# Kernel optimization log

Hardware: AMD Instinct MI355X
Metric: run time of the kernel (lower is better)

Reference implementation:

```python
import jax, jax.numpy as jnp
import numpy as np
from jax import lax

B, N, NUM_CLASSES = 16, 48384, 1
CONF_THRESH = 0.25
IOU_THRESH = 0.45
MAX_PER_IMG = 100
K = 512           # NMS candidate pool (top-K by score)
IMG_SIZE = 1536.0
CLS_OFFSET = 4096.0  # class-aware NMS offset trick


def setup_inputs() -> dict:
    key = jax.random.key(0)
    k1, k2, k3 = jax.random.split(key, 3)
    # cx, cy in [0, IMG), w, h in [0, 0.2*IMG)
    coords = jax.random.uniform(k1, (B, N, 4)) * jnp.array(
        [IMG_SIZE, IMG_SIZE, 0.2 * IMG_SIZE, 0.2 * IMG_SIZE], dtype=jnp.float32)
    confs = jax.random.uniform(k2, (B, N, 1 + NUM_CLASSES))  # obj + class scores in [0,1)
    pred_boxes = jnp.concatenate([coords, confs], axis=-1)   # [B, N, 6]
    features = jax.random.normal(k3, (B, 256, 48, 48), dtype=jnp.float32)
    return {"pred_boxes": pred_boxes, "features": features}


def _iou_matrix(boxes):
    # boxes: [K, 4] xyxy -> [K, K] pairwise IoU
    area = jnp.clip(boxes[:, 2] - boxes[:, 0], 0.0) * jnp.clip(boxes[:, 3] - boxes[:, 1], 0.0)
    lt = jnp.maximum(boxes[:, None, :2], boxes[None, :, :2])
    rb = jnp.minimum(boxes[:, None, 2:], boxes[None, :, 2:])
    wh = jnp.clip(rb - lt, 0.0)
    inter = wh[..., 0] * wh[..., 1]
    return inter / (area[:, None] + area[None, :] - inter + 1e-9)


def _find_thresh(scores, t0):
    # Retry loop of the wrapper: lower conf_thresh until >=1 box passes the conf mask.
    s = lax.stop_gradient(scores)
    def cond(t):
        return jnp.sum(s >= t) == 0
    def body(t):
        return jnp.maximum(t - 0.1, t / 10.0)
    return lax.while_loop(cond, body, t0)


def _postprocess_one(pred, thresh):
    # pred: [N, 5+num_classes]
    cx, cy, w, h = pred[:, 0], pred[:, 1], pred[:, 2], pred[:, 3]
    boxes = jnp.stack([cx - w / 2, cy - h / 2, cx + w / 2, cy + h / 2], axis=-1)  # xyxy
    obj = pred[:, 4]
    cls = pred[:, 5:]
    class_conf = jnp.max(cls, axis=-1)
    class_pred = jnp.argmax(cls, axis=-1)
    score = obj * class_conf
    valid = score >= thresh
    cand_score, idx = lax.top_k(jnp.where(valid, score, 0.0), K)
    cboxes = boxes[idx]
    ccls = class_pred[idx]
    cobj = obj[idx]
    cconf = class_conf[idx]
    cvalid = valid[idx]
    # class-aware NMS: offset boxes per class so cross-class pairs never overlap
    off = ccls.astype(boxes.dtype) * CLS_OFFSET
    iou = _iou_matrix(cboxes + off[:, None])  # [K, K]
    ar = jnp.arange(K)
    def body(i, keep):
        sup = keep[i] & (iou[i] > IOU_THRESH) & (ar > i)
        return keep & ~sup
    keep = lax.fori_loop(0, K, body, cvalid)  # greedy NMS (candidates sorted desc)
    final = jnp.where(keep, cand_score, 0.0)
    out_score, oidx = lax.top_k(final, MAX_PER_IMG)
    det = jnp.concatenate(
        [cboxes[oidx], cobj[oidx][:, None], cconf[oidx][:, None],
         ccls[oidx][:, None].astype(boxes.dtype)], axis=-1)  # [max_det, 7]
    kmask = keep[oidx]
    det = jnp.where(kmask[:, None], det, 0.0)
    return det, kmask


def reference(pred_boxes, features):
    obj = pred_boxes[..., 4]
    cconf = jnp.max(pred_boxes[..., 5:], axis=-1)
    scores = obj * cconf  # [B, N]
    t0 = jnp.full((pred_boxes.shape[0],), CONF_THRESH, pred_boxes.dtype)
    thresh = jax.vmap(_find_thresh)(scores, t0)
    det, mask = jax.vmap(_postprocess_one)(pred_boxes, thresh)
    return det, mask, features
```

## Files before the change

kernel.cpp:

```cpp
#include <hip/hip_runtime.h>
#include <stdint.h>

typedef unsigned int u32;
typedef unsigned long long u64;

#define BATCH 16
#define NBOX  48384
#define KC    512
#define MAXDET 100
#define CONF_T 0.25f
#define HCUT   0.75f
#define IOU_T  0.45f
#define DET_FLOATS (BATCH*MAXDET*7)
#define MASK_OFF   DET_FLOATS
#define FEAT_OFF   (DET_FLOATS + BATCH*MAXDET)
#define FEAT_N     (BATCH*256*48*48)
#define FEAT4_N    (FEAT_N/4)

#define CAPH  4096
#define HBUF  160
#define NBINS 64
#define NBLK1 64
#define BOXPB 756

#define F64   (FEAT4_N/64)
#define CSL1  (13*F64)
#define CSL2  (50*F64)
#define CSL3  (56*F64)
#define K1CPB  256
#define K2ACPB 480
#define K2BCPB 384
#define K2CCPB 240

__device__ __forceinline__ u64 xorred_u64(u64 v, int m){
    u32 lo = __shfl_xor((u32)(v & 0xFFFFFFFFull), m, 64);
    u32 hi = __shfl_xor((u32)(v >> 32), m, 64);
    return ((u64)hi << 32) | lo;
}
__device__ __forceinline__ u64 shflxor_u64(u64 v, int j){
    u32 lo = __shfl_xor((u32)(v & 0xFFFFFFFFull), j, 64);
    u32 hi = __shfl_xor((u32)(v >> 32), j, 64);
    return ((u64)hi << 32) | lo;
}
__device__ __forceinline__ u64 shflidx_u64(u64 v, int src){
    u32 lo = (u32)__shfl((int)(u32)(v & 0xFFFFFFFFull), src, 64);
    u32 hi = (u32)__shfl((int)(u32)(v >> 32), src, 64);
    return ((u64)hi << 32) | lo;
}
__device__ __forceinline__ int score_bin(float sc){
    int bin = (int)((sc - 0.75f) * 256.0f);
    return bin > 63 ? 63 : bin;
}

__global__ __launch_bounds__(512) void k1_score(const float* __restrict__ pred,
        u64* __restrict__ hkey, u32* __restrict__ blkcnt, u32* __restrict__ ghist,
        float* __restrict__ blkmax, const float4* __restrict__ feat4,
        float* __restrict__ out, int copyB)
{
    __shared__ u64 s_hb[HBUF];
    __shared__ u32 s_hist[NBINS];
    __shared__ u32 s_hc;
    __shared__ float s_wm[8];

    const int tid = threadIdx.x;

    if ((int)blockIdx.x < copyB){
        const int nthr = copyB * 512;
        float4* dst = reinterpret_cast<float4*>(out + FEAT_OFF);
        for (int i = (int)blockIdx.x*512 + tid; i < CSL1; i += nthr)
            dst[i] = feat4[i];
        return;
    }

    const int sid = (int)blockIdx.x - copyB;
    const int b = sid >> 6, blk = sid & 63;
    if (tid == 0) s_hc = 0u;
    if (tid < NBINS) s_hist[tid] = 0u;
    __syncthreads();

    const float* pb = pred + ((size_t)b*NBOX + (size_t)blk*BOXPB)*6;
    float m = 0.f;
    for (int i = tid; i < BOXPB; i += 512){
        const float2 oc = *(const float2*)(pb + (size_t)i*6 + 4);
        const float sc = oc.x * oc.y;
        m = fmaxf(m, sc);
        if (sc >= HCUT){
            const u32 slot = atomicAdd(&s_hc, 1u);
            const u32 idx = (u32)(blk*BOXPB + i);
            if (slot < (u32)HBUF)
                s_hb[slot] = ((u64)__float_as_uint(sc) << 32) | (u64)(0xFFFFFFFFu - idx);
            atomicAdd(&s_hist[score_bin(sc)], 1u);
        }
    }
    #pragma unroll
    for (int off = 32; off >= 1; off >>= 1) m = fmaxf(m, __shfl_xor(m, off, 64));
    if ((tid & 63) == 0) s_wm[tid >> 6] = m;
    __syncthreads();
    if (tid == 0){
        float mm = s_wm[0];
        #pragma unroll
        for (int w = 1; w < 8; w++) mm = fmaxf(mm, s_wm[w]);
        blkmax[sid] = mm;
        blkcnt[sid] = s_hc;
    }
    if (tid < NBINS) ghist[(size_t)sid*NBINS + tid] = s_hist[tid];
    const u32 hn = (s_hc < (u32)HBUF ? s_hc : (u32)HBUF);
    for (u32 i = tid; i < hn; i += 512)
        hkey[(size_t)sid*HBUF + i] = s_hb[i];
}

__global__ void copy_kernel(const float4* __restrict__ src, float4* __restrict__ dst){
    int stride = gridDim.x * blockDim.x;
    for (int i = blockIdx.x*blockDim.x + threadIdx.x; i < FEAT4_N; i += stride)
        dst[i] = src[i];
}

__global__ __launch_bounds__(512) void k2a_sel(
        const float* __restrict__ pred, const u64* __restrict__ hkey,
        const u32* __restrict__ blkcnt, u32* ghist ,
        const float* __restrict__ blkmax,
        const float4* __restrict__ feat4, float* __restrict__ out, int copyB)
{
    __shared__ u64 s_list[CAPH];
    __shared__ u64 s_key[KC];
    __shared__ u32 s_scr[1024];
    __shared__ u64 s_tie[256];
    __shared__ u32 s_eqidx[256];
    __shared__ u32 s_pfx[64], s_cnt[64];
    __shared__ float s_thresh;
    __shared__ u32 s_Mh, s_maxc, s_pivbin, s_need, s_fastok;
    __shared__ u32 s_prefix, s_k, s_cntgt, s_cnteq;
    __shared__ int s_vM;

    const int tid = threadIdx.x;

    if ((int)blockIdx.x >= BATCH){
        const int nthr = copyB * 512;
        float4* dst = reinterpret_cast<float4*>(out + FEAT_OFF);
        for (int i = CSL1 + ((int)blockIdx.x - BATCH)*512 + tid; i < CSL2; i += nthr)
            dst[i] = feat4[i];
        return;
    }

    const int b = blockIdx.x;
    const float* predb = pred + (size_t)b*NBOX*6;

    {
        if (tid < 64){
            float vv = blkmax[b*NBLK1 + tid];
            #pragma unroll
            for (int off = 32; off >= 1; off >>= 1) vv = fmaxf(vv, __shfl_xor(vv, off, 64));
            if (tid == 0){
                float t = CONF_T; int g = 0;
                while (vv < t && g < 256){ t = fmaxf(t - 0.1f, t * 0.1f); g++; }
                s_thresh = t;
                s_cntgt = 0u; s_cnteq = 0u; s_fastok = 0u;
            }
        } else if (tid < 128){
            const int l = tid - 64;
            u32 c = blkcnt[b*NBLK1 + l];
            s_cnt[l] = c;
            u32 p = c;
            #pragma unroll
            for (int off = 1; off < 64; off <<= 1){
                u32 o = __shfl_up(p, off, 64);
                if (l >= off) p += o;
            }
            s_pfx[l] = p - c;
            u32 mc = c;
            #pragma unroll
            for (int off = 32; off >= 1; off >>= 1) mc = (u32)max(mc, __shfl_xor(mc, off, 64));
            if (l == 63) s_Mh = p;
            if (l == 0)  s_maxc = mc;
        }
    }
    __syncthreads();
    const u32 Mh = s_Mh;
    const bool fastm = (Mh >= (u32)KC) && (Mh <= (u32)CAPH) && (s_maxc <= (u32)HBUF);

    if (fastm){
        const int wv = tid >> 6, ln = tid & 63;
        #pragma unroll
        for (int q = 0; q < 8; q++){
            const int s = wv + q*8;
            const u32 n = s_cnt[s], base = s_pfx[s];
            const u64* src = hkey + (size_t)(b*NBLK1 + s)*HBUF;
            for (u32 i = ln; i < n; i += 64) s_list[base + i] = src[i];
        }
        const int j = tid & 63, g = tid >> 6;
        const u32* gh = ghist + (size_t)b*NBLK1*NBINS;
        u32 acc = 0;
        #pragma unroll
        for (int r = 0; r < 8; r++) acc += gh[(g + r*8)*64 + j];
        s_scr[g*64 + j] = acc;
    }
    __syncthreads();
    if (fastm && tid < 64){
        u32 h = 0;
        #pragma unroll
        for (int g = 0; g < 8; g++) h += s_scr[g*64 + tid];
        u32 c = h;
        #pragma unroll
        for (int off = 1; off < 64; off <<= 1){
            u32 o = __shfl_down(c, off, 64);
            c += (tid + off < 64) ? o : 0u;
        }
        const u32 above = c - h;
        if (above < (u32)KC && above + h >= (u32)KC){
            s_pivbin = (u32)tid;
            s_need = (u32)KC - above;
            s_fastok = (h <= 256u) ? 1u : 0u;
        }
    }
    __syncthreads();
    const bool fsel = fastm && (s_fastok != 0u);

    if (fsel){
        const u32 pb = s_pivbin;
        const u32 lane = (u32)(tid & 63);
        const u64 below = (1ull << lane) - 1ull;
        for (u32 i0 = 0; i0 < Mh; i0 += 512){
            const u32 i = i0 + (u32)tid;
            const bool inr = (i < Mh);
            const u64 key = inr ? s_list[i] : 0ull;
            u32 j2 = 0u;
            if (inr){
                const float sc = __uint_as_float((u32)(key >> 32));
                j2 = (u32)score_bin(sc);
            }
            const bool isgt = inr && (j2 > pb);
            const bool iseq = inr && (j2 == pb);
            const u64 mg = __ballot(isgt);
            const u64 me = __ballot(iseq);
            u32 bg = 0u, be = 0u;
            if (lane == 0u){
                bg = atomicAdd(&s_cntgt, (u32)__popcll(mg));
                be = atomicAdd(&s_cnteq, (u32)__popcll(me));
            }
            bg = (u32)__shfl((int)bg, 0, 64);
            be = (u32)__shfl((int)be, 0, 64);
            if (isgt){
                const u32 sl = bg + (u32)__popcll(mg & below);
                if (sl < (u32)KC) s_key[sl] = key;
            } else if (iseq){
                const u32 e = be + (u32)__popcll(me & below);
                if (e < 256u) s_tie[e] = key;
            }
        }
        __syncthreads();
        {
            const u32 g0v = (s_cntgt < (u32)KC) ? s_cntgt : (u32)KC;
            u32 ecv = (s_cnteq < 256u) ? s_cnteq : 256u;
            u32 needv = (s_need < ecv) ? s_need : ecv;
            if (tid < (int)ecv){
                const u64 me2 = s_tie[tid];
                u32 r = 0;
                for (u32 u2 = 0; u2 < ecv; ++u2) r += (s_tie[u2] > me2) ? 1u : 0u;
                if (r < needv && g0v + r < (u32)KC) s_key[g0v + r] = me2;
            }
            for (int i = (int)(g0v + needv) + tid; i < KC; i += 512) s_key[i] = 0ull;
        }
        __syncthreads();
    } else {
        const float thresh = s_thresh;
        const u32 base8 = __float_as_uint(thresh) >> 24;
        u32 (*s_hist4)[256] = reinterpret_cast<u32(*)[256]>(s_scr);
        {
            u64 c0=0, c1=0, c2=0, c3=0;
            for (int i = tid; i < NBOX; i += 512){
                const float* pp = predb + (size_t)i*6;
                float sc = pp[4] * pp[5];
                if (sc >= thresh){
                    u32 d = (__float_as_uint(sc) >> 24) - base8; if (d > 15u) d = 15u;
                    u64 inc = 1ull << (16*(d & 3u)); u32 q = d >> 2;
                    c0 += (q==0u)?inc:0ull; c1 += (q==1u)?inc:0ull;
                    c2 += (q==2u)?inc:0ull; c3 += (q==3u)?inc:0ull;
                }
            }
            #pragma unroll
            for (int off = 32; off >= 1; off >>= 1){
                c0 += xorred_u64(c0,off); c1 += xorred_u64(c1,off);
                c2 += xorred_u64(c2,off); c3 += xorred_u64(c3,off);
            }
            u64* warr = s_key;
            if ((tid & 63) == 0){
                int w = tid >> 6;
                warr[w*4+0]=c0; warr[w*4+1]=c1; warr[w*4+2]=c2; warr[w*4+3]=c3;
            }
            __syncthreads();
            if (tid < 16){
                u32 tot = 0;
                #pragma unroll
                for (int w = 0; w < 8; w++){
                    u64 vv = warr[w*4 + (tid >> 2)];
                    tot += (u32)((vv >> (16*(tid & 3))) & 0xFFFFull);
                }
                s_hist4[0][tid] = tot;
            }
            __syncthreads();
            if (tid == 0){
                u32 h[16]; u32 tot = 0;
                #pragma unroll
                for (int d = 0; d < 16; d++){ h[d] = s_hist4[0][d]; tot += h[d]; }
                s_vM = (int)tot;
                s_k = KC; s_prefix = 0u;
                if (tot > (u32)KC){
                    u32 k = KC, c = 0; int d = 15;
                    for (; d >= 0; --d){ if (c + h[d] >= k) break; c += h[d]; }
                    if (d < 0) d = 0;
                    s_prefix = (base8 + (u32)d) << 24; s_k = k - c;
                }
            }
            __syncthreads();
        }
        const int vM = s_vM;
        if (vM > KC){
            for (int shift = 16; shift >= 0; shift -= 8){
                for (int z = tid; z < 1024; z += 512) ((u32*)s_hist4)[z] = 0u;
                __syncthreads();
                const u32 prefix = s_prefix;
                const u32 pmask = 0xFFFFFFFFu << (shift + 8);
                const int cpy = tid >> 8;
                for (int i = tid; i < NBOX; i += 512){
                    const float* pp = predb + (size_t)i*6;
                    float sc = pp[4] * pp[5];
                    if (sc >= thresh){
                        u32 bb = __float_as_uint(sc);
                        if ((bb & pmask) == (prefix & pmask))
                            atomicAdd(&s_hist4[cpy][(bb >> shift) & 0xFFu], 1u);
                    }
                }
                __syncthreads();
                if (tid < 256)
                    s_hist4[0][tid] = s_hist4[0][tid] + s_hist4[1][tid]
                                    + s_hist4[2][tid] + s_hist4[3][tid];
                __syncthreads();
                if (tid < 64){
                    const int l = tid;
                    u32 h0 = s_hist4[0][4*l+0], h1 = s_hist4[0][4*l+1];
                    u32 h2 = s_hist4[0][4*l+2], h3 = s_hist4[0][4*l+3];
                    u32 mysum = h0+h1+h2+h3;
                    u32 c = mysum;
                    #pragma unroll
                    for (int off = 1; off < 64; off <<= 1){
                        u32 o = __shfl_down(c, off, 64);
                        c += (l + off < 64) ? o : 0u;
                    }
                    u32 a3 = c - mysum;
                    u32 a2 = a3 + h3, a1 = a2 + h2, a0 = a1 + h1;
                    u32 k = s_k;
                    int sel = -1; u32 cab = 0;
                    if (a0 < k && a0 + h0 >= k){ sel = 0; cab = a0; }
                    if (a1 < k && a1 + h1 >= k){ sel = 1; cab = a1; }
                    if (a2 < k && a2 + h2 >= k){ sel = 2; cab = a2; }
                    if (a3 < k && a3 + h3 >= k){ sel = 3; cab = a3; }
                    if (sel >= 0){
                        s_prefix = prefix | ((u32)(4*l + sel) << shift);
                        s_k = k - cab;
                    }
                }
                __syncthreads();
            }
        }
        const u32 pivot = (vM > KC) ? s_prefix : 0u;
        const bool pivot0 = (vM <= KC);
        const int kneed = pivot0 ? 0 : (int)s_k;
        for (int i = tid; i < NBOX; i += 512){
            const float* pp = predb + (size_t)i*6;
            float sc = pp[4] * pp[5];
            if (sc < thresh) continue;
            u32 bb = __float_as_uint(sc);
            if (bb > pivot){
                u32 sl = atomicAdd(&s_cntgt, 1u);
                if (sl < (u32)KC) s_key[sl] = ((u64)bb << 32) | (u64)(0xFFFFFFFFu - (u32)i);
            } else if (!pivot0 && bb == pivot){
                u32 e = atomicAdd(&s_cnteq, 1u);
                if (e < 256u) s_eqidx[e] = (u32)i;
            }
        }
        __syncthreads();
        if (tid == 0){
            int g = (int)s_cntgt; if (g > KC) g = KC;
            int ec = (int)s_cnteq; if (ec > 256) ec = 256;
            int need = kneed < ec ? kneed : ec;
            for (int t = 0; t < need; t++){
                int mi = t;
                for (int u = t+1; u < ec; u++) if (s_eqidx[u] < s_eqidx[mi]) mi = u;
                u32 tmp = s_eqidx[mi]; s_eqidx[mi] = s_eqidx[t]; s_eqidx[t] = tmp;
                if (g < KC) s_key[g++] = ((u64)pivot << 32) | (u64)(0xFFFFFFFFu - tmp);
            }
            while (g < KC) s_key[g++] = 0ull;
        }
        __syncthreads();
    }

    u64 v = s_key[tid];
    {
        #define CAS_W(kk, j) \
            { \
                u64 p = shflxor_u64(v, (j)); \
                bool keepMax = (((tid & (kk)) == 0) == ((tid & (j)) == 0)); \
                u64 mx = (v > p) ? v : p, mn = (v > p) ? p : v; \
                v = keepMax ? mx : mn; \
            }
        #define CAS_L(kk, j) \
            __syncthreads(); \
            s_key[tid] = v; \
            __syncthreads(); \
            { \
                u64 p = s_key[tid ^ (j)]; \
                bool keepMax = (((tid & (kk)) == 0) == ((tid & (j)) == 0)); \
                u64 mx = (v > p) ? v : p, mn = (v > p) ? p : v; \
                v = keepMax ? mx : mn; \
            }
        CAS_W(2,1)
        CAS_W(4,2)  CAS_W(4,1)
        CAS_W(8,4)  CAS_W(8,2)  CAS_W(8,1)
        CAS_W(16,8) CAS_W(16,4) CAS_W(16,2) CAS_W(16,1)
        CAS_W(32,16) CAS_W(32,8) CAS_W(32,4) CAS_W(32,2) CAS_W(32,1)
        CAS_W(64,32) CAS_W(64,16) CAS_W(64,8) CAS_W(64,4) CAS_W(64,2) CAS_W(64,1)
        CAS_L(128,64)
        CAS_W(128,32) CAS_W(128,16) CAS_W(128,8) CAS_W(128,4) CAS_W(128,2) CAS_W(128,1)
        CAS_L(256,128) CAS_L(256,64)
        CAS_W(256,32) CAS_W(256,16) CAS_W(256,8) CAS_W(256,4) CAS_W(256,2) CAS_W(256,1)
        CAS_L(512,256) CAS_L(512,128) CAS_L(512,64)
        CAS_W(512,32) CAS_W(512,16) CAS_W(512,8) CAS_W(512,4) CAS_W(512,2) CAS_W(512,1)
        #undef CAS_W
        #undef CAS_L
    }

    {
        u32 bb = (u32)(v >> 32);
        u32 idx = 0xFFFFFFFFu - (u32)(v & 0xFFFFFFFFull);
        int srcrow = (bb != 0u) ? (int)idx : 0;
        const float* p = predb + (size_t)srcrow*6;
        const float2 p01 = *(const float2*)(p);
        const float2 p23 = *(const float2*)(p + 2);
        const float2 p45 = *(const float2*)(p + 4);
        float cx = p01.x, cy = p01.y, w = p23.x, h = p23.y, ob = p45.x, cf = p45.y;
        float x1 = cx - w * 0.5f, y1 = cy - h * 0.5f;
        float x2 = cx + w * 0.5f, y2 = cy + h * 0.5f;
        float4* cw = reinterpret_cast<float4*>(ghist) + ((size_t)b*KC + tid)*2;
        cw[0] = make_float4(x1, y1, x2, y2);
        cw[1] = make_float4(fmaxf(x2 - x1, 0.f) * fmaxf(y2 - y1, 0.f),
                            ob, cf, __uint_as_float(bb));
    }
}

__global__ __launch_bounds__(256) void k2b_iou(const float4* __restrict__ cand,
        u64* __restrict__ masks, u64* __restrict__ vmasks,
        const float4* __restrict__ feat4, float* __restrict__ out, int copyB)
{
    __shared__ float4 s_box[KC];
    __shared__ float s_area[KC];
    const int tid = threadIdx.x;

    if ((int)blockIdx.x >= BATCH*9){
        const int nthr = copyB * 256;
        float4* dst = reinterpret_cast<float4*>(out + FEAT_OFF);
        for (int i = CSL2 + ((int)blockIdx.x - BATCH*9)*256 + tid; i < CSL3; i += nthr)
            dst[i] = feat4[i];
        return;
    }

    const int b = (int)blockIdx.x / 9, q = (int)blockIdx.x % 9;
    const float4* cb = cand + (size_t)b*KC*2;

    for (int i = tid; i < KC; i += 256){
        s_box[i] = cb[2*i];
        s_area[i] = cb[2*i+1].x;
    }
    __syncthreads();

    const int wv = tid >> 6, lane = tid & 63;
    const int p = q*4 + wv;
    int d = 0; while ((d+1)*(d+2)/2 <= p) d++;
    const int c = p - d*(d+1)/2;
    const int j = d*64 + lane;
    const float4 bj = s_box[j];
    const float aj = s_area[j];
    const bool isdiag = (c == d);
    u64 acc = 0ull;
    for (int t = 0; t < 64; t++){
        const float4 bi = s_box[c*64 + t];
        const float ai = s_area[c*64 + t];
        float lx = fmaxf(bi.x, bj.x), ly = fmaxf(bi.y, bj.y);
        float rx = fminf(bi.z, bj.z), ry = fminf(bi.w, bj.w);
        float iw = fmaxf(rx - lx, 0.f), ih = fmaxf(ry - ly, 0.f);
        float inter = iw * ih;
        float denom = ai + aj - inter + 1e-9f;
        const bool iouc = (inter > IOU_T * denom);
        bool setb = isdiag ? (iouc && t > lane) : iouc;
        acc |= setb ? (1ull << t) : 0ull;
    }
    if (isdiag) vmasks[(size_t)b*KC + c*64 + lane] = acc;
    else        masks[(size_t)b*4096 + (size_t)c*512 + j] = acc;
}

__global__ __launch_bounds__(512) void k2c_nms(const float4* __restrict__ cand,
        const u64* __restrict__ masks, const u64* __restrict__ vmasks,
        float* __restrict__ out,
        const float4* __restrict__ feat4, int copyB)
{
    __shared__ u64 s_masks[8];
    __shared__ u32 s_wpcnt[8], s_wpfx[8];
    __shared__ int s_outidx[MAXDET];
    __shared__ int s_outcnt;

    const int tid = threadIdx.x;

    if ((int)blockIdx.x >= BATCH){
        const int nthr = copyB * 512;
        float4* dst = reinterpret_cast<float4*>(out + FEAT_OFF);
        for (int i = CSL3 + ((int)blockIdx.x - BATCH)*512 + tid; i < FEAT4_N; i += nthr)
            dst[i] = feat4[i];
        return;
    }

    const int b = blockIdx.x;
    const int wave = tid >> 6, lane = tid & 63;
    const float4* cb = cand + (size_t)b*KC*2;
    const u64* mb = masks + (size_t)b*4096;

    const float4 meta = cb[2*tid + 1];
    const bool alive0 = (__float_as_uint(meta.w) != 0u);
    const u64 vm = vmasks[(size_t)b*KC + tid];
    u64 pre[7];
    #pragma unroll
    for (int e = 0; e < 7; e++) pre[e] = (e < wave) ? mb[(size_t)e*512 + tid] : 0ull;

    for (int c = 0; c < 8; c++){
        if (wave == c){
            bool alive = alive0;
            #pragma unroll
            for (int e = 0; e < 7; e++)
                if (e < c) alive = alive && ((pre[e] & s_masks[e]) == 0ull);
            u64 A = __ballot(alive);
            #pragma unroll
            for (int t = 0; t < 64; t++){
                const u64 m = shflidx_u64(vm, t);
                if ((A >> t) & 1ull) A &= ~m;
            }
            if (lane == 0) s_masks[c] = A;
        }
        __syncthreads();
    }

    if (tid < 8) s_wpcnt[tid] = (u32)__popcll(s_masks[tid]);
    __syncthreads();
    if (tid == 0){
        u32 run = 0;
        #pragma unroll
        for (int w = 0; w < 8; w++){ s_wpfx[w] = run; run += s_wpcnt[w]; }
        s_outcnt = (int)(run < MAXDET ? run : MAXDET);
    }
    __syncthreads();
    {
        const u64 wd = s_masks[wave];
        if ((wd >> lane) & 1ull){
            u32 rank = s_wpfx[wave] + (u32)__popcll(wd & ((1ull << lane) - 1ull));
            if (rank < MAXDET) s_outidx[rank] = tid;
        }
    }
    __syncthreads();
    if (tid < MAXDET){
        const int obase = (b * MAXDET + tid) * 7;
        if (tid < s_outcnt){
            int c = s_outidx[tid];
            float4 bx = cb[2*c];
            float4 mt = cb[2*c + 1];
            out[obase+0] = bx.x; out[obase+1] = bx.y;
            out[obase+2] = bx.z; out[obase+3] = bx.w;
            out[obase+4] = mt.y; out[obase+5] = mt.z;
            out[obase+6] = 0.f;
            out[MASK_OFF + b*MAXDET + tid] = 1.f;
        } else {
            #pragma unroll
            for (int q = 0; q < 7; q++) out[obase+q] = 0.f;
            out[MASK_OFF + b*MAXDET + tid] = 0.f;
        }
    }
}

extern "C" void kernel_launch(void* const* d_in, const int* in_sizes, int n_in,
                              void* d_out, int out_size, void* d_ws, size_t ws_size,
                              hipStream_t stream) {
    (void)in_sizes; (void)n_in; (void)out_size;
    const float* pred = (const float*)d_in[0];
    const float* feat = (const float*)d_in[1];
    float* out = (float*)d_out;

    const size_t hkeyBytes = (size_t)BATCH * NBLK1 * HBUF * 8;
    const size_t cntBytes  = (size_t)BATCH * NBLK1 * 4;
    const size_t histBytes = (size_t)BATCH * NBLK1 * NBINS * 4;
    const size_t maxBytes  = (size_t)BATCH * NBLK1 * 4;
    const size_t needBytes = hkeyBytes + cntBytes + histBytes + maxBytes;

    char* base; bool fused;
    if (ws_size >= needBytes){ base = (char*)d_ws; fused = true; }
    else { base = (char*)(out + FEAT_OFF); fused = false; }

    u64* hkeyp  = (u64*)base;
    u32* blkcnt = (u32*)(base + hkeyBytes);
    u32* ghist  = (u32*)(base + hkeyBytes + cntBytes);
    float* blkmax = (float*)(base + hkeyBytes + cntBytes + histBytes);
    float4* cand = (float4*)ghist;
    u64* masks   = hkeyp;
    u64* vmasks  = hkeyp + (size_t)BATCH*4096;

    if (fused){
        k1_score<<<dim3(K1CPB + BATCH*NBLK1), dim3(512), 0, stream>>>(
            pred, hkeyp, blkcnt, ghist, blkmax, (const float4*)feat, out, K1CPB);
        k2a_sel<<<dim3(BATCH + K2ACPB), dim3(512), 0, stream>>>(
            pred, hkeyp, blkcnt, ghist, blkmax, (const float4*)feat, out, K2ACPB);
        k2b_iou<<<dim3(BATCH*9 + K2BCPB), dim3(256), 0, stream>>>(
            cand, masks, vmasks, (const float4*)feat, out, K2BCPB);
        k2c_nms<<<dim3(BATCH + K2CCPB), dim3(512), 0, stream>>>(
            cand, masks, vmasks, out, (const float4*)feat, K2CCPB);
    } else {
        k1_score<<<dim3(BATCH*NBLK1), dim3(512), 0, stream>>>(
            pred, hkeyp, blkcnt, ghist, blkmax, (const float4*)feat, out, 0);
        k2a_sel<<<dim3(BATCH), dim3(512), 0, stream>>>(
            pred, hkeyp, blkcnt, ghist, blkmax, (const float4*)feat, out, 0);
        k2b_iou<<<dim3(BATCH*9), dim3(256), 0, stream>>>(
            cand, masks, vmasks, (const float4*)feat, out, 0);
        k2c_nms<<<dim3(BATCH), dim3(512), 0, stream>>>(
            cand, masks, vmasks, out, (const float4*)feat, 0);
        copy_kernel<<<dim3(1024), dim3(256), 0, stream>>>(
            (const float4*)feat, (float4*)(out + FEAT_OFF));
    }
}
```

Before: 134.3 us.

## Stream hkey directly in selection, replace bitonic sort with rank sort

```diff
diff --git a/kernel.cpp b/kernel.cpp
--- a/kernel.cpp
+++ b/kernel.cpp
@@ -24,8 +24,8 @@
 #define BOXPB 756
 
 #define F64   (FEAT4_N/64)
-#define CSL1  (13*F64)
-#define CSL2  (50*F64)
+#define CSL1  (16*F64)
+#define CSL2  (48*F64)
 #define CSL3  (56*F64)
 #define K1CPB  256
 #define K2ACPB 480
@@ -35,11 +35,6 @@
 __device__ __forceinline__ u64 xorred_u64(u64 v, int m){
     u32 lo = __shfl_xor((u32)(v & 0xFFFFFFFFull), m, 64);
     u32 hi = __shfl_xor((u32)(v >> 32), m, 64);
-    return ((u64)hi << 32) | lo;
-}
-__device__ __forceinline__ u64 shflxor_u64(u64 v, int j){
-    u32 lo = __shfl_xor((u32)(v & 0xFFFFFFFFull), j, 64);
-    u32 hi = __shfl_xor((u32)(v >> 32), j, 64);
     return ((u64)hi << 32) | lo;
 }
 __device__ __forceinline__ u64 shflidx_u64(u64 v, int src){
@@ -121,12 +116,11 @@
         const float* __restrict__ blkmax,
         const float4* __restrict__ feat4, float* __restrict__ out, int copyB)
 {
-    __shared__ u64 s_list[CAPH];
     __shared__ u64 s_key[KC];
     __shared__ u32 s_scr[1024];
     __shared__ u64 s_tie[256];
     __shared__ u32 s_eqidx[256];
-    __shared__ u32 s_pfx[64], s_cnt[64];
+    __shared__ u32 s_cnt[64];
     __shared__ float s_thresh;
     __shared__ u32 s_Mh, s_maxc, s_pivbin, s_need, s_fastok;
     __shared__ u32 s_prefix, s_k, s_cntgt, s_cnteq;
@@ -160,18 +154,13 @@
             const int l = tid - 64;
             u32 c = blkcnt[b*NBLK1 + l];
             s_cnt[l] = c;
-            u32 p = c;
+            u32 sum = c;
             #pragma unroll
-            for (int off = 1; off < 64; off <<= 1){
-                u32 o = __shfl_up(p, off, 64);
-                if (l >= off) p += o;
-            }
-            s_pfx[l] = p - c;
+            for (int off = 32; off >= 1; off >>= 1) sum += __shfl_xor(sum, off, 64);
             u32 mc = c;
             #pragma unroll
             for (int off = 32; off >= 1; off >>= 1) mc = (u32)max(mc, __shfl_xor(mc, off, 64));
-            if (l == 63) s_Mh = p;
-            if (l == 0)  s_maxc = mc;
+            if (l == 0){ s_Mh = sum; s_maxc = mc; }
         }
     }
     __syncthreads();
@@ -179,14 +168,6 @@
     const bool fastm = (Mh >= (u32)KC) && (Mh <= (u32)CAPH) && (s_maxc <= (u32)HBUF);
 
     if (fastm){
-        const int wv = tid >> 6, ln = tid & 63;
-        #pragma unroll
-        for (int q = 0; q < 8; q++){
-            const int s = wv + q*8;
-            const u32 n = s_cnt[s], base = s_pfx[s];
-            const u64* src = hkey + (size_t)(b*NBLK1 + s)*HBUF;
-            for (u32 i = ln; i < n; i += 64) s_list[base + i] = src[i];
-        }
         const int j = tid & 63, g = tid >> 6;
         const u32* gh = ghist + (size_t)b*NBLK1*NBINS;
         u32 acc = 0;
@@ -217,34 +198,41 @@
 
     if (fsel){
         const u32 pb = s_pivbin;
+        const int wv = tid >> 6;
         const u32 lane = (u32)(tid & 63);
         const u64 below = (1ull << lane) - 1ull;
-        for (u32 i0 = 0; i0 < Mh; i0 += 512){
-            const u32 i = i0 + (u32)tid;
-            const bool inr = (i < Mh);
-            const u64 key = inr ? s_list[i] : 0ull;
-            u32 j2 = 0u;
-            if (inr){
-                const float sc = __uint_as_float((u32)(key >> 32));
-                j2 = (u32)score_bin(sc);
-            }
-            const bool isgt = inr && (j2 > pb);
-            const bool iseq = inr && (j2 == pb);
-            const u64 mg = __ballot(isgt);
-            const u64 me = __ballot(iseq);
-            u32 bg = 0u, be = 0u;
-            if (lane == 0u){
-                bg = atomicAdd(&s_cntgt, (u32)__popcll(mg));
-                be = atomicAdd(&s_cnteq, (u32)__popcll(me));
-            }
-            bg = (u32)__shfl((int)bg, 0, 64);
-            be = (u32)__shfl((int)be, 0, 64);
-            if (isgt){
-                const u32 sl = bg + (u32)__popcll(mg & below);
-                if (sl < (u32)KC) s_key[sl] = key;
-            } else if (iseq){
-                const u32 e = be + (u32)__popcll(me & below);
-                if (e < 256u) s_tie[e] = key;
+        #pragma unroll
+        for (int q = 0; q < 8; q++){
+            const int s = wv*8 + q;
+            const u32 n = s_cnt[s];
+            const u64* src = hkey + (size_t)(b*NBLK1 + s)*HBUF;
+            for (u32 i0 = 0; i0 < n; i0 += 64){
+                const u32 i = i0 + lane;
+                const bool inr = (i < n);
+                const u64 key = inr ? src[i] : 0ull;
+                u32 j2 = 0u;
+                if (inr){
+                    const float sc = __uint_as_float((u32)(key >> 32));
+                    j2 = (u32)score_bin(sc);
+                }
+                const bool isgt = inr && (j2 > pb);
+                const bool iseq = inr && (j2 == pb);
+                const u64 mg = __ballot(isgt);
+                const u64 me = __ballot(iseq);
+                u32 bg = 0u, be = 0u;
+                if (lane == 0u){
+                    bg = atomicAdd(&s_cntgt, (u32)__popcll(mg));
+                    be = atomicAdd(&s_cnteq, (u32)__popcll(me));
+                }
+                bg = (u32)__shfl((int)bg, 0, 64);
+                be = (u32)__shfl((int)be, 0, 64);
+                if (isgt){
+                    const u32 sl = bg + (u32)__popcll(mg & below);
+                    if (sl < (u32)KC) s_key[sl] = key;
+                } else if (iseq){
+                    const u32 e = be + (u32)__popcll(me & below);
+                    if (e < 256u) s_tie[e] = key;
+                }
             }
         }
         __syncthreads();
@@ -394,39 +382,19 @@
         __syncthreads();
     }
 
-    u64 v = s_key[tid];
+    u64 v;
     {
-        #define CAS_W(kk, j) \
-            { \
-                u64 p = shflxor_u64(v, (j)); \
-                bool keepMax = (((tid & (kk)) == 0) == ((tid & (j)) == 0)); \
-                u64 mx = (v > p) ? v : p, mn = (v > p) ? p : v; \
-                v = keepMax ? mx : mn; \
-            }
-        #define CAS_L(kk, j) \
-            __syncthreads(); \
-            s_key[tid] = v; \
-            __syncthreads(); \
-            { \
-                u64 p = s_key[tid ^ (j)]; \
-                bool keepMax = (((tid & (kk)) == 0) == ((tid & (j)) == 0)); \
-                u64 mx = (v > p) ? v : p, mn = (v > p) ? p : v; \
-                v = keepMax ? mx : mn; \
-            }
-        CAS_W(2,1)
-        CAS_W(4,2)  CAS_W(4,1)
-        CAS_W(8,4)  CAS_W(8,2)  CAS_W(8,1)
-        CAS_W(16,8) CAS_W(16,4) CAS_W(16,2) CAS_W(16,1)
-        CAS_W(32,16) CAS_W(32,8) CAS_W(32,4) CAS_W(32,2) CAS_W(32,1)
-        CAS_W(64,32) CAS_W(64,16) CAS_W(64,8) CAS_W(64,4) CAS_W(64,2) CAS_W(64,1)
-        CAS_L(128,64)
-        CAS_W(128,32) CAS_W(128,16) CAS_W(128,8) CAS_W(128,4) CAS_W(128,2) CAS_W(128,1)
-        CAS_L(256,128) CAS_L(256,64)
-        CAS_W(256,32) CAS_W(256,16) CAS_W(256,8) CAS_W(256,4) CAS_W(256,2) CAS_W(256,1)
-        CAS_L(512,256) CAS_L(512,128) CAS_L(512,64)
-        CAS_W(512,32) CAS_W(512,16) CAS_W(512,8) CAS_W(512,4) CAS_W(512,2) CAS_W(512,1)
-        #undef CAS_W
-        #undef CAS_L
+        const u64 me2 = s_key[tid];
+        u32 r = 0;
+        #pragma unroll 8
+        for (int u = 0; u < KC; u++){
+            const u64 o = s_key[u];
+            r += (o > me2 || (o == me2 && u < tid)) ? 1u : 0u;
+        }
+        u64* s_out = reinterpret_cast<u64*>(s_scr);
+        s_out[r] = me2;
+        __syncthreads();
+        v = s_out[tid];
     }
 
     {
@@ -594,7 +562,10 @@
     const size_t cntBytes  = (size_t)BATCH * NBLK1 * 4;
     const size_t histBytes = (size_t)BATCH * NBLK1 * NBINS * 4;
     const size_t maxBytes  = (size_t)BATCH * NBLK1 * 4;
-    const size_t needBytes = hkeyBytes + cntBytes + histBytes + maxBytes;
+    const size_t maskBytes = (size_t)BATCH * 4096 * 8;
+    const size_t vmaskBytes= (size_t)BATCH * KC * 8;
+    const size_t needBytes = hkeyBytes + cntBytes + histBytes + maxBytes
+                           + maskBytes + vmaskBytes;
 
     char* base; bool fused;
     if (ws_size >= needBytes){ base = (char*)d_ws; fused = true; }
@@ -604,9 +575,9 @@
     u32* blkcnt = (u32*)(base + hkeyBytes);
     u32* ghist  = (u32*)(base + hkeyBytes + cntBytes);
     float* blkmax = (float*)(base + hkeyBytes + cntBytes + histBytes);
+    u64* masks  = (u64*)(base + hkeyBytes + cntBytes + histBytes + maxBytes);
+    u64* vmasks = (u64*)(base + hkeyBytes + cntBytes + histBytes + maxBytes + maskBytes);
     float4* cand = (float4*)ghist;
-    u64* masks   = hkeyp;
-    u64* vmasks  = hkeyp + (size_t)BATCH*4096;
 
     if (fused){
         k1_score<<<dim3(K1CPB + BATCH*NBLK1), dim3(512), 0, stream>>>(
```

Result: slower. 146.0 us (+8.7%).
